# Kernel optimization log

Hardware: AMD Instinct MI355X
Metric: run time of the kernel (lower is better)

## Reference

```python
import jax, jax.numpy as jnp
import numpy as np

N, E, D, H, G, L, EF = 50000, 800000, 128, 256, 512, 3, 8
BN_EPS = 1e-5


def _bn(h, g, b):
    # torch BatchNorm1d in training mode: biased batch stats over the node axis
    m = h.mean(0)
    v = h.var(0)
    return g * (h - m) * jax.lax.rsqrt(v + BN_EPS) + b


def setup_inputs() -> dict:
    ks = jax.random.split(jax.random.key(0), 12)
    sc = 0.05
    return {
        "x": jax.random.normal(ks[0], (N, D), jnp.float32),
        "edge_attr": jax.random.normal(ks[1], (E, EF), jnp.float32),
        "vn_emb": jnp.zeros((1, D), jnp.float32),  # init.constant_(0)
        "We": jax.random.normal(ks[2], (L, EF, D)) * sc,
        "be": jnp.zeros((L, D)),
        "W1": jax.random.normal(ks[3], (L, D, H)) * sc,
        "b1": jnp.zeros((L, H)),
        "g1": jnp.ones((L, H)),
        "bt1": jnp.zeros((L, H)),
        "W2": jax.random.normal(ks[4], (L, H, D)) * sc,
        "b2": jnp.zeros((L, D)),
        "gb": jnp.ones((L, D)),
        "bb": jnp.zeros((L, D)),
        "Wv1": jax.random.normal(ks[5], (L - 1, D, H)) * sc,
        "bv1": jnp.zeros((L - 1, H)),
        "gv1": jnp.ones((L - 1, H)),
        "btv1": jnp.zeros((L - 1, H)),
        "Wv2": jax.random.normal(ks[6], (L - 1, H, D)) * sc,
        "bv2": jnp.zeros((L - 1, D)),
        "gv2": jnp.ones((L - 1, D)),
        "btv2": jnp.zeros((L - 1, D)),
        "edge_index": jax.random.randint(ks[7], (2, E), 0, N),
        "batch": jnp.sort(jax.random.randint(ks[8], (N,), 0, G)),
    }


def reference(x, edge_attr, vn_emb, We, be, W1, b1, g1, bt1, W2, b2, gb, bb,
              Wv1, bv1, gv1, btv1, Wv2, bv2, gv2, btv2, edge_index, batch):
    src, dst = edge_index[0], edge_index[1]
    vn = jnp.broadcast_to(vn_emb, (G, D))  # Embedding(1, D) looked up for every graph
    h = x  # node_encoder is None -> encoded_node = x
    for l in range(L):
        h_in = h + vn[batch]                              # virtual-node broadcast (gather)
        e = edge_attr @ We[l] + be[l]                     # per-layer edge encoder
        msg = jax.nn.relu(h_in[src] + e)                  # GIN message, [E, D]
        aggr = jax.ops.segment_sum(msg, dst, num_segments=N)
        z = h_in + aggr                                   # (1+eps)*h + aggr, eps=0
        z = jax.nn.relu(_bn(z @ W1[l] + b1[l], g1[l], bt1[l]))
        h = _bn(z @ W2[l] + b2[l], gb[l], bb[l])          # conv MLP out + outer BatchNorm
        if l < L - 1:
            h = jax.nn.relu(h)                            # dropout ratio 0 -> identity
            pooled = jax.ops.segment_sum(h_in, batch, num_segments=G) + vn
            t = jax.nn.relu(_bn(pooled @ Wv1[l] + bv1[l], gv1[l], btv1[l]))
            vn = jax.nn.relu(_bn(t @ Wv2[l] + bv2[l], gv2[l], btv2[l]))
    return h  # JK == 'last'
```

## Files before the change

### kernel.cpp

```cpp
#include <hip/hip_runtime.h>
#include <hip/hip_bf16.h>

#define N_NODES 50000
#define N_EDGES 800000
#define DIM 128
#define HID 256
#define N_GRAPH 512
#define N_LAYER 3
#define EFEAT 8
#define BN_EPS 1e-5f
#define MAX_GROUPS 240000
#define AGGR_WAVES 8192
#define SCAN_BLOCKS ((N_NODES + 1023) / 1024)

typedef unsigned short u16;
typedef unsigned int u32;

using bf16x8_t = short __attribute__((ext_vector_type(8)));
using f32x4_t  = float __attribute__((ext_vector_type(4)));
using f32x2    = float __attribute__((ext_vector_type(2)));
using f32x4v   = float __attribute__((ext_vector_type(4)));


__device__ __forceinline__ void atomic_add_f(float* p, float v) {
    unsafeAtomicAdd(p, v);
}
__device__ __forceinline__ u16 f2bf(float x) {
    union { float f; u32 u; } v; v.f = x;
    u32 r = v.u + 0x7FFF + ((v.u >> 16) & 1);
    return (u16)(r >> 16);
}
__device__ __forceinline__ float bf2f(u16 u) {
    union { u32 i; float f; } v; v.i = (u32)u << 16; return v.f;
}
__device__ __forceinline__ float2 up2(u32 p) {
    return make_float2(bf2f((u16)(p & 0xFFFF)), bf2f((u16)(p >> 16)));
}
__device__ __forceinline__ u32 pk2(float a, float b) {
    return (u32)f2bf(a) | ((u32)f2bf(b) << 16);
}
__device__ __forceinline__ f32x2 up2p(u32 p) {
    union { u32 u[2]; f32x2 f; } v;
    v.u[0] = p << 16;
    v.u[1] = p & 0xFFFF0000u;
    return v.f;
}
__device__ __forceinline__ f32x2 splat2(float x) {
    f32x2 r; r.x = x; r.y = x; return r;
}

__global__ __launch_bounds__(256) void wconv_kernel(
    const float* __restrict__ W1, const float* __restrict__ W2,
    u16* __restrict__ W1t, u16* __restrict__ W2t)
{
    int idx = blockIdx.x * 256 + threadIdx.x;
    if (idx >= 6 * 32768) return;
    int m = idx >> 15;
    int off = idx & 32767;
    int l = m >> 1;
    if ((m & 1) == 0) {
        int r = off >> 8, c = off & 255;
        W1t[(size_t)l * 32768 + c * 128 + r] = f2bf(W1[(size_t)l * 32768 + r * 256 + c]);
    } else {
        int r = off >> 7, c = off & 127;
        W2t[(size_t)l * 32768 + c * 256 + r] = f2bf(W2[(size_t)l * 32768 + r * 128 + c]);
    }
}

__global__ __launch_bounds__(256) void hist_rank_kernel(
    const int* __restrict__ ei, int* __restrict__ deg, int* __restrict__ rank)
{
    int e = blockIdx.x * 256 + threadIdx.x;
    if (e >= N_EDGES) return;
    int dst = ei[N_EDGES + e];
    rank[e] = atomicAdd(&deg[dst], 1);
}

__global__ __launch_bounds__(1024) void scan1_kernel(
    const int* __restrict__ deg, int* __restrict__ grpptr, int* __restrict__ bsum)
{
    __shared__ int wsum[16];
    int blk = blockIdx.x, tid = threadIdx.x;
    int i = blk * 1024 + tid;
    int v = (i < N_NODES) ? ((deg[i] + 3) >> 2) : 0;
    int lane = tid & 63, w = tid >> 6;
    int s = v;
    #pragma unroll
    for (int d = 1; d < 64; d <<= 1) { int t = __shfl_up(s, d); if (lane >= d) s += t; }
    if (lane == 63) wsum[w] = s;
    __syncthreads();
    if (tid < 64) {
        int t = (tid < 16) ? wsum[tid] : 0;
        #pragma unroll
        for (int d = 1; d < 16; d <<= 1) { int u = __shfl_up(t, d); if (tid >= d) t += u; }
        if (tid < 16) wsum[tid] = t;
    }
    __syncthreads();
    int excl = (w > 0) ? wsum[w - 1] : 0;
    int incl = s + excl;
    if (i < N_NODES) grpptr[i + 1] = incl;
    if (tid == 1023) bsum[blk] = incl;
}

__global__ __launch_bounds__(64) void scan2_kernel(int* __restrict__ bsum) {
    int tid = threadIdx.x;
    int v = (tid < SCAN_BLOCKS) ? bsum[tid] : 0;
    int s = v;
    #pragma unroll
    for (int d = 1; d < 64; d <<= 1) { int t = __shfl_up(s, d); if (tid >= d) s += t; }
    if (tid < SCAN_BLOCKS) bsum[tid] = s - v;
}

__global__ __launch_bounds__(1024) void scan3_kernel(
    int* __restrict__ grpptr, const int* __restrict__ bsum)
{
    int blk = blockIdx.x;
    int i = blk * 1024 + threadIdx.x;
    if (i < N_NODES) grpptr[i + 1] += bsum[blk];
    if (blk == 0 && threadIdx.x == 0) grpptr[0] = 0;
}

__global__ __launch_bounds__(256) void padinit_kernel(
    uint4* __restrict__ rec4, int nq, u16* __restrict__ hin)
{
    int i = blockIdx.x * 256 + threadIdx.x;
    if (blockIdx.x == 0 && threadIdx.x < 64)
        *(u32*)(hin + (size_t)N_NODES * DIM + threadIdx.x * 2) = 0xFF7FFF7Fu;
    if (i >= nq) return;
    u32 s = (u32)N_NODES << 8;
    rec4[i] = make_uint4(s, 0u, s, 0u);
}

__global__ __launch_bounds__(256) void scatter_kernel(
    const int* __restrict__ ei,
    const int* __restrict__ rank, const int* __restrict__ grpptr,
    uint2* __restrict__ srec)
{
    int e = blockIdx.x * 256 + threadIdx.x;
    if (e >= N_EDGES) return;
    int src = __builtin_nontemporal_load(ei + e);
    int dst = __builtin_nontemporal_load(ei + N_EDGES + e);
    int rk  = __builtin_nontemporal_load(rank + e);
    int slot = (grpptr[dst] + (rk >> 2)) * 4 + (rk & 3);
    uint2 v;
    v.x = (u32)src << 8;
    v.y = (u32)e << 5;
    srec[slot] = v;
}

__global__ __launch_bounds__(256) void expand_kernel(
    const uint2* __restrict__ srec, const float* __restrict__ ea,
    char* __restrict__ brec, int nslots)
{
    int i = blockIdx.x * 256 + threadIdx.x;
    if (i >= nslots) return;
    int g = i >> 2;
    int j = i & 3;
    uint2 v = srec[i];
    const char* eaB = (const char*)ea;
    f32x4v lo = *(const f32x4v*)(eaB + v.y);
    f32x4v hi = *(const f32x4v*)(eaB + v.y + 16);
    char* rb = brec + (size_t)g * 144;
    *(u32*)(rb + j * 4) = v.x;
    *(f32x4v*)(rb + 16 + j * 32) = lo;
    *(f32x4v*)(rb + 32 + j * 32) = hi;
}

__global__ __launch_bounds__(256) void wstart_kernel(
    const int* __restrict__ grpptr, int* __restrict__ wstart)
{
    int w = blockIdx.x * 256 + threadIdx.x;
    if (w > AGGR_WAVES) return;
    if (w == AGGR_WAVES) { wstart[w] = N_NODES; return; }
    int Gt = grpptr[N_NODES];
    int q = (int)(((long long)w * Gt) / AGGR_WAVES);
    int lo = 0, hi = N_NODES;
    while (lo < hi) { int mid = (lo + hi) >> 1; if (grpptr[mid] < q) lo = mid + 1; else hi = mid; }
    wstart[w] = lo;
}

template <bool USEBN, int VNM>
__global__ __launch_bounds__(256) void hin_kernel(
    const float* __restrict__ src,
    const float* __restrict__ sum2, const float* __restrict__ ss2,
    const float* __restrict__ g, const float* __restrict__ b, float invN,
    const int* __restrict__ batch,
    const float* __restrict__ vn_emb,
    const float* __restrict__ vnpre, const float* __restrict__ vsum, const float* __restrict__ vss,
    const float* __restrict__ gv, const float* __restrict__ btv, float invG,
    u16* __restrict__ hin, int total4)
{
    int idx = blockIdx.x * 256 + threadIdx.x;
    if (idx >= total4) return;
    int base = idx * 4;
    int n = base >> 7;
    int c = base & (DIM - 1);
    float4 v = *(const float4*)(src + base);
    float o[4] = {v.x, v.y, v.z, v.w};
    if (USEBN) {
        #pragma unroll
        for (int j = 0; j < 4; ++j) {
            int cj = c + j;
            float m = sum2[cj] * invN;
            float var = ss2[cj] * invN - m * m;
            float r = rsqrtf(var + BN_EPS);
            float a = g[cj] * r;
            o[j] = fmaxf(fmaf(a, o[j], b[cj] - m * a), 0.f);
        }
    }
    int grp = batch[n];
    if (VNM == 0) {
        const float4 w = *(const float4*)(vn_emb + c);
        o[0] += w.x; o[1] += w.y; o[2] += w.z; o[3] += w.w;
    } else {
        const float4 vp = *(const float4*)(vnpre + (size_t)grp * DIM + c);
        float vv[4] = {vp.x, vp.y, vp.z, vp.w};
        #pragma unroll
        for (int j = 0; j < 4; ++j) {
            int cj = c + j;
            float m = vsum[cj] * invG;
            float var = vss[cj] * invG - m * m;
            float r = rsqrtf(var + BN_EPS);
            float a = gv[cj] * r;
            o[j] += fmaxf(fmaf(a, vv[j], btv[cj] - m * a), 0.f);
        }
    }
    uint2 pk;
    pk.x = pk2(o[0], o[1]);
    pk.y = pk2(o[2], o[3]);
    *(uint2*)(hin + base) = pk;
}

__device__ __forceinline__ void edge_term_f(
    u32 h, f32x4v ea, f32x4v eb, const f32x2* rW, f32x2 rB, f32x2& acc)
{
    f32x2 ex = rB;
    ex = __builtin_elementwise_fma(splat2(ea.x), rW[0], ex);
    ex = __builtin_elementwise_fma(splat2(ea.y), rW[1], ex);
    ex = __builtin_elementwise_fma(splat2(ea.z), rW[2], ex);
    ex = __builtin_elementwise_fma(splat2(ea.w), rW[3], ex);
    ex = __builtin_elementwise_fma(splat2(eb.x), rW[4], ex);
    ex = __builtin_elementwise_fma(splat2(eb.y), rW[5], ex);
    ex = __builtin_elementwise_fma(splat2(eb.z), rW[6], ex);
    ex = __builtin_elementwise_fma(splat2(eb.w), rW[7], ex);
    f32x2 s = up2p(h) + ex;
    s = __builtin_elementwise_max(s, splat2(0.f));
    acc += s;
}

__global__ __launch_bounds__(256) void aggr_kernel(
    const int* __restrict__ grpptr, const char* __restrict__ rec,
    const float* __restrict__ Wel, const float* __restrict__ bel,
    const u16* __restrict__ hin, u16* __restrict__ z,
    const int* __restrict__ wstart, float* __restrict__ stats)
{
    const int lane = threadIdx.x & 63;
    const int cb = lane * 4;
    const int wid = __builtin_amdgcn_readfirstlane((blockIdx.x << 2) + (threadIdx.x >> 6));

    if (blockIdx.x == 0) {
        #pragma unroll
        for (int i = 0; i < 8; ++i) stats[i * 256 + threadIdx.x] = 0.f;
    }

    f32x2 rW[EFEAT];
    #pragma unroll
    for (int k = 0; k < EFEAT; ++k) {
        float2 t = *(const float2*)(Wel + k * DIM + lane * 2);
        rW[k].x = t.x; rW[k].y = t.y;
    }
    float2 tb = *(const float2*)(bel + lane * 2);
    f32x2 rB; rB.x = tb.x; rB.y = tb.y;

    const char* hinB = (const char*)hin;
    int n = wstart[wid];
    const int n1 = wstart[wid + 1];

    while (n < n1 && grpptr[n + 1] == grpptr[n]) {
        f32x2 a0 = up2p(*(const u32*)(hinB + ((u32)n << 8) + cb));
        *(u32*)(z + ((size_t)n << 7) + lane * 2) = pk2(a0.x, a0.y);
        ++n;
    }
    if (n < n1) {
        int g = grpptr[n];
        const int gTot = grpptr[n1];
        int gEnd = grpptr[n + 1];
        f32x2 acc = up2p(*(const u32*)(hinB + ((u32)n << 8) + cb));
        const char* rb = rec + (size_t)g * 144;

        uint4 so = *(const uint4*)rb;
        u32 h0 = *(const u32*)(hinB + so.x + cb);
        u32 h1 = *(const u32*)(hinB + so.y + cb);
        u32 h2 = *(const u32*)(hinB + so.z + cb);
        u32 h3 = *(const u32*)(hinB + so.w + cb);
        f32x4v e0a = *(const f32x4v*)(rb + 16);
        f32x4v e0b = *(const f32x4v*)(rb + 32);
        f32x4v e1a = *(const f32x4v*)(rb + 48);
        f32x4v e1b = *(const f32x4v*)(rb + 64);
        f32x4v e2a = *(const f32x4v*)(rb + 80);
        f32x4v e2b = *(const f32x4v*)(rb + 96);
        f32x4v e3a = *(const f32x4v*)(rb + 112);
        f32x4v e3b = *(const f32x4v*)(rb + 128);
        uint4 soN = *(const uint4*)(rb + 144);

        #pragma unroll 2
        for (; g < gTot; ++g, rb += 144) {
            u32 i0 = *(const u32*)(hinB + soN.x + cb);
            u32 i1 = *(const u32*)(hinB + soN.y + cb);
            u32 i2 = *(const u32*)(hinB + soN.z + cb);
            u32 i3 = *(const u32*)(hinB + soN.w + cb);
            f32x4v f0a = *(const f32x4v*)(rb + 160);
            f32x4v f0b = *(const f32x4v*)(rb + 176);
            f32x4v f1a = *(const f32x4v*)(rb + 192);
            f32x4v f1b = *(const f32x4v*)(rb + 208);
            f32x4v f2a = *(const f32x4v*)(rb + 224);
            f32x4v f2b = *(const f32x4v*)(rb + 240);
            f32x4v f3a = *(const f32x4v*)(rb + 256);
            f32x4v f3b = *(const f32x4v*)(rb + 272);
            uint4 soNN = *(const uint4*)(rb + 288);
            edge_term_f(h0, e0a, e0b, rW, rB, acc);
            edge_term_f(h1, e1a, e1b, rW, rB, acc);
            edge_term_f(h2, e2a, e2b, rW, rB, acc);
            edge_term_f(h3, e3a, e3b, rW, rB, acc);
            h0 = i0; h1 = i1; h2 = i2; h3 = i3;
            e0a = f0a; e0b = f0b; e1a = f1a; e1b = f1b;
            e2a = f2a; e2b = f2b; e3a = f3a; e3b = f3b;
            soN = soNN;
            if (g + 1 == gEnd) {
                *(u32*)(z + ((size_t)n << 7) + lane * 2) = pk2(acc.x, acc.y);
                ++n;
                if (g + 1 < gTot) {
                    while (grpptr[n + 1] == grpptr[n]) {
                        f32x2 a0 = up2p(*(const u32*)(hinB + ((u32)n << 8) + cb));
                        *(u32*)(z + ((size_t)n << 7) + lane * 2) = pk2(a0.x, a0.y);
                        ++n;
                    }
                    acc = up2p(*(const u32*)(hinB + ((u32)n << 8) + cb));
                    gEnd = grpptr[n + 1];
                }
            }
        }
    }
    while (n < n1) {
        f32x2 a0 = up2p(*(const u32*)(hinB + ((u32)n << 8) + cb));
        *(u32*)(z + ((size_t)n << 7) + lane * 2) = pk2(a0.x, a0.y);
        ++n;
    }
}

template <int MODE, bool CBF16>
__global__ __launch_bounds__(256) void gemm_bf16_kernel(
    const u16* __restrict__ Aa,
    const float* __restrict__ sSum, const float* __restrict__ sSS,
    const float* __restrict__ gA, const float* __restrict__ btA, float invCnt,
    const u16* __restrict__ Bt,
    const float* __restrict__ bias,
    void* __restrict__ CoutV,
    float* __restrict__ outSum, float* __restrict__ outSS,
    int M, int K, int Nc)
{
    constexpr int BM = 128, BN = 128, BK = 128;
    constexpr int LDA = BK + 8;
    __shared__ u16 As[BM * LDA];
    __shared__ u16 Bs[64 * LDA];
    __shared__ float csum[BN], css[BN];

    const int tid = threadIdx.x;
    const int wave = tid >> 6, lane = tid & 63;
    const int row0 = blockIdx.x * BM, col0 = blockIdx.y * BN;
    const int w_m = (wave & 1) * 64, w_n = (wave >> 1) * 32;
    const int quad = lane >> 4, l16 = lane & 15;

    if (tid < BN) { csum[tid] = 0.f; css[tid] = 0.f; }

    f32x4_t acc[4][4];
    #pragma unroll
    for (int mi = 0; mi < 4; ++mi)
        #pragma unroll
        for (int ni = 0; ni < 4; ++ni)
            acc[mi][ni] = (f32x4_t){0.f, 0.f, 0.f, 0.f};

    const int kc = (tid & 15) * 8;
    const int nkt = K / BK;

    for (int kt = 0; kt < nkt; ++kt) {
        float af[8], bf_[8];
        if (MODE == 1) {
            #pragma unroll
            for (int j = 0; j < 8; ++j) {
                int kg = kt * BK + kc + j;
                float m = sSum[kg] * invCnt;
                float var = sSS[kg] * invCnt - m * m;
                float r = rsqrtf(var + BN_EPS);
                float a = gA[kg] * r;
                af[j] = a;
                bf_[j] = btA[kg] - m * a;
            }
        }
        #pragma unroll
        for (int it = 0; it < 8; ++it) {
            int chunk = it * 256 + tid;
            int row = chunk >> 4;
            int gr = row0 + row; if (gr >= M) gr = M - 1;
            uint4 q = *(const uint4*)(Aa + (size_t)gr * K + kt * BK + kc);
            if (MODE == 1) {
                float2 p0 = up2(q.x), p1 = up2(q.y), p2 = up2(q.z), p3 = up2(q.w);
                p0.x = fmaxf(fmaf(af[0], p0.x, bf_[0]), 0.f);
                p0.y = fmaxf(fmaf(af[1], p0.y, bf_[1]), 0.f);
                p1.x = fmaxf(fmaf(af[2], p1.x, bf_[2]), 0.f);
                p1.y = fmaxf(fmaf(af[3], p1.y, bf_[3]), 0.f);
                p2.x = fmaxf(fmaf(af[4], p2.x, bf_[4]), 0.f);
                p2.y = fmaxf(fmaf(af[5], p2.y, bf_[5]), 0.f);
                p3.x = fmaxf(fmaf(af[6], p3.x, bf_[6]), 0.f);
                p3.y = fmaxf(fmaf(af[7], p3.y, bf_[7]), 0.f);
                q.x = pk2(p0.x, p0.y); q.y = pk2(p1.x, p1.y);
                q.z = pk2(p2.x, p2.y); q.w = pk2(p3.x, p3.y);
            }
            *(uint4*)(As + row * LDA + kc) = q;
        }
        #pragma unroll
        for (int half = 0; half < 2; ++half) {
            #pragma unroll
            for (int it = 0; it < 4; ++it) {
                int chunk = it * 256 + tid;
                int n = chunk >> 4;
                uint4 q = *(const uint4*)(Bt + (size_t)(col0 + half * 64 + n) * K + kt * BK + kc);
                *(uint4*)(Bs + n * LDA + kc) = q;
            }
            __syncthreads();
            #pragma unroll
            for (int ks = 0; ks < 4; ++ks) {
                bf16x8_t a_frag[4], b_frag[2];
                #pragma unroll
                for (int mi = 0; mi < 4; ++mi)
                    a_frag[mi] = *(const bf16x8_t*)(As + (w_m + mi * 16 + l16) * LDA + ks * 32 + quad * 8);
                #pragma unroll
                for (int ni = 0; ni < 2; ++ni)
                    b_frag[ni] = *(const bf16x8_t*)(Bs + (w_n + ni * 16 + l16) * LDA + ks * 32 + quad * 8);
                #pragma unroll
                for (int mi = 0; mi < 4; ++mi)
                    #pragma unroll
                    for (int ni = 0; ni < 2; ++ni)
                        acc[mi][half * 2 + ni] = __builtin_amdgcn_mfma_f32_16x16x32_bf16(
                            a_frag[mi], b_frag[ni], acc[mi][half * 2 + ni], 0, 0, 0);
            }
            __syncthreads();
        }
    }

    u16* Cb = (u16*)CoutV;
    float* Cf = (float*)CoutV;
    #pragma unroll
    for (int half = 0; half < 2; ++half)
    #pragma unroll
    for (int ni = 0; ni < 2; ++ni) {
        int ccol = half * 64 + w_n + ni * 16 + l16;
        int col = col0 + ccol;
        float bv = bias[col];
        float s = 0.f, qs = 0.f;
        #pragma unroll
        for (int mi = 0; mi < 4; ++mi) {
            int rbase = row0 + w_m + mi * 16 + quad * 4;
            #pragma unroll
            for (int reg = 0; reg < 4; ++reg) {
                int gr = rbase + reg;
                if (gr < M) {
                    float o = acc[mi][half * 2 + ni][reg] + bv;
                    s += o;
                    qs += o * o;
                    if (CBF16) Cb[(size_t)gr * Nc + col] = f2bf(o);
                    else       Cf[(size_t)gr * Nc + col] = o;
                }
            }
        }
        s += __shfl_xor(s, 16);  s += __shfl_xor(s, 32);
        qs += __shfl_xor(qs, 16);  qs += __shfl_xor(qs, 32);
        if (quad == 0) {
            atomicAdd(&csum[ccol], s);
            atomicAdd(&css[ccol], qs);
        }
    }
    __syncthreads();
    if (tid < BN) {
        atomic_add_f(outSum + col0 + tid, csum[tid]);
        atomic_add_f(outSS + col0 + tid, css[tid]);
    }
}

template <int MODE>
__global__ __launch_bounds__(256) void gemm_kernel(
    const float* __restrict__ Aa,
    const float* __restrict__ sSum, const float* __restrict__ sSS,
    const float* __restrict__ gA, const float* __restrict__ btA, float invCnt,
    const float* __restrict__ B, const float* __restrict__ bias,
    float* __restrict__ Cout, float* __restrict__ outSum, float* __restrict__ outSS,
    int M, int K, int Nc)
{
    __shared__ float As[16][68];
    __shared__ float Bs[16][64];
    __shared__ float alphaS[256], betaS[256];
    __shared__ float csum[64], css[64];

    const int tid = threadIdx.x;
    const int tx = tid & 15, ty = tid >> 4;
    const int row0 = blockIdx.x * 64, col0 = blockIdx.y * 64;

    if (tid < 64) { csum[tid] = 0.f; css[tid] = 0.f; }
    if (MODE == 1) {
        for (int k = tid; k < K; k += 256) {
            float m = sSum[k] * invCnt;
            float var = sSS[k] * invCnt - m * m;
            float r = rsqrtf(var + BN_EPS);
            float a = gA[k] * r;
            alphaS[k] = a;
            betaS[k] = btA[k] - m * a;
        }
    }
    __syncthreads();

    float acc[4][4];
    #pragma unroll
    for (int i = 0; i < 4; ++i)
        #pragma unroll
        for (int j = 0; j < 4; ++j) acc[i][j] = 0.f;

    const int lr = tid >> 2;
    const int lk = (tid & 3) * 4;
    const int bk = tid >> 4;
    const int bc = tx * 4;

    for (int kt = 0; kt < K; kt += 16) {
        int gr = row0 + lr;
        float4 va = make_float4(0.f, 0.f, 0.f, 0.f);
        if (gr < M) {
            va = *(const float4*)(Aa + (size_t)gr * K + kt + lk);
            if (MODE == 1) {
                int k0 = kt + lk;
                va.x = fmaxf(fmaf(alphaS[k0 + 0], va.x, betaS[k0 + 0]), 0.f);
                va.y = fmaxf(fmaf(alphaS[k0 + 1], va.y, betaS[k0 + 1]), 0.f);
                va.z = fmaxf(fmaf(alphaS[k0 + 2], va.z, betaS[k0 + 2]), 0.f);
                va.w = fmaxf(fmaf(alphaS[k0 + 3], va.w, betaS[k0 + 3]), 0.f);
            }
        }
        As[lk + 0][lr] = va.x;
        As[lk + 1][lr] = va.y;
        As[lk + 2][lr] = va.z;
        As[lk + 3][lr] = va.w;
        const float4 vb4 = *(const float4*)(B + (size_t)(kt + bk) * Nc + col0 + bc);
        *(float4*)&Bs[bk][bc] = vb4;
        __syncthreads();
        #pragma unroll
        for (int kk = 0; kk < 16; ++kk) {
            const float4 a4 = *(const float4*)&As[kk][ty * 4];
            const float4 b4 = *(const float4*)&Bs[kk][tx * 4];
            float av[4] = {a4.x, a4.y, a4.z, a4.w};
            float bv4[4] = {b4.x, b4.y, b4.z, b4.w};
            #pragma unroll
            for (int i = 0; i < 4; ++i)
                #pragma unroll
                for (int j = 0; j < 4; ++j)
                    acc[i][j] = fmaf(av[i], bv4[j], acc[i][j]);
        }
        __syncthreads();
    }

    const float4 bvv = *(const float4*)(bias + col0 + tx * 4);
    float bias4[4] = {bvv.x, bvv.y, bvv.z, bvv.w};
    float ps[4] = {0.f, 0.f, 0.f, 0.f};
    float pq[4] = {0.f, 0.f, 0.f, 0.f};
    #pragma unroll
    for (int i = 0; i < 4; ++i) {
        int gr = row0 + ty * 4 + i;
        if (gr < M) {
            float o[4];
            #pragma unroll
            for (int j = 0; j < 4; ++j) {
                o[j] = acc[i][j] + bias4[j];
                ps[j] += o[j];
                pq[j] += o[j] * o[j];
            }
            *(float4*)(Cout + (size_t)gr * Nc + col0 + tx * 4) = make_float4(o[0], o[1], o[2], o[3]);
        }
    }
    #pragma unroll
    for (int j = 0; j < 4; ++j) {
        atomicAdd(&csum[tx * 4 + j], ps[j]);
        atomicAdd(&css[tx * 4 + j], pq[j]);
    }
    __syncthreads();
    if (tid < 64) {
        atomic_add_f(outSum + col0 + tid, csum[tid]);
        atomic_add_f(outSS + col0 + tid, css[tid]);
    }
}

template <int VNM>
__global__ __launch_bounds__(64) void pooled_seg_kernel(
    const u16* __restrict__ hin, const int* __restrict__ batch,
    const float* __restrict__ vn_emb,
    const float* __restrict__ vnpre, const float* __restrict__ vsum, const float* __restrict__ vss,
    const float* __restrict__ gv, const float* __restrict__ btv, float invG,
    float* __restrict__ pooled)
{
    int g = blockIdx.x;
    int lane = threadIdx.x;
    int c2 = lane * 2;
    int lo = 0, hi = N_NODES;
    while (lo < hi) { int mid = (lo + hi) >> 1; if (batch[mid] < g) lo = mid + 1; else hi = mid; }
    int start = lo;
    hi = N_NODES;
    while (lo < hi) { int mid = (lo + hi) >> 1; if (batch[mid] < g + 1) lo = mid + 1; else hi = mid; }
    int end = lo;

    f32x2 acc;
    if (VNM == 0) {
        float2 w = *(const float2*)(vn_emb + c2);
        acc.x = w.x; acc.y = w.y;
    } else {
        float2 vs = *(const float2*)(vsum + c2);
        float2 vq = *(const float2*)(vss + c2);
        float2 gg = *(const float2*)(gv + c2);
        float2 bt = *(const float2*)(btv + c2);
        float2 vp = *(const float2*)(vnpre + (size_t)g * DIM + c2);
        float m0 = vs.x * invG, m1 = vs.y * invG;
        float va0 = vq.x * invG - m0 * m0, va1 = vq.y * invG - m1 * m1;
        float a0 = gg.x * rsqrtf(va0 + BN_EPS), a1 = gg.y * rsqrtf(va1 + BN_EPS);
        acc.x = fmaxf(fmaf(a0, vp.x, bt.x - m0 * a0), 0.f);
        acc.y = fmaxf(fmaf(a1, vp.y, bt.y - m1 * a1), 0.f);
    }

    const char* hinB = (const char*)hin;
    const int cb = lane * 4;
    f32x2 s0 = splat2(0.f), s1 = splat2(0.f), s2 = splat2(0.f), s3 = splat2(0.f);
    int n = start;
    for (; n + 3 < end; n += 4) {
        s0 += up2p(*(const u32*)(hinB + ((size_t)(n + 0) << 8) + cb));
        s1 += up2p(*(const u32*)(hinB + ((size_t)(n + 1) << 8) + cb));
        s2 += up2p(*(const u32*)(hinB + ((size_t)(n + 2) << 8) + cb));
        s3 += up2p(*(const u32*)(hinB + ((size_t)(n + 3) << 8) + cb));
    }
    for (; n < end; ++n) s0 += up2p(*(const u32*)(hinB + ((size_t)n << 8) + cb));
    acc += (s0 + s1) + (s2 + s3);
    *(float2*)(pooled + (size_t)g * DIM + c2) = make_float2(acc.x, acc.y);
}

__global__ __launch_bounds__(256) void final_bn_kernel(
    float* __restrict__ outp, const float* __restrict__ sum2, const float* __restrict__ ss2,
    const float* __restrict__ g, const float* __restrict__ b, float invN, int total4)
{
    int idx = blockIdx.x * 256 + threadIdx.x;
    if (idx >= total4) return;
    int base = idx * 4;
    int c = base & (DIM - 1);
    float4 v = *(const float4*)(outp + base);
    float o[4] = {v.x, v.y, v.z, v.w};
    #pragma unroll
    for (int j = 0; j < 4; ++j) {
        int cj = c + j;
        float m = sum2[cj] * invN;
        float var = ss2[cj] * invN - m * m;
        float r = rsqrtf(var + BN_EPS);
        float a = g[cj] * r;
        o[j] = fmaf(a, o[j], b[cj] - m * a);
    }
    *(float4*)(outp + base) = make_float4(o[0], o[1], o[2], o[3]);
}

extern "C" void kernel_launch(void* const* d_in, const int* in_sizes, int n_in,
                              void* d_out, int out_size, void* d_ws, size_t ws_size,
                              hipStream_t stream) {
    const float* x         = (const float*)d_in[0];
    const float* edge_attr = (const float*)d_in[1];
    const float* vn_emb    = (const float*)d_in[2];
    const float* We        = (const float*)d_in[3];
    const float* be        = (const float*)d_in[4];
    const float* W1        = (const float*)d_in[5];
    const float* b1        = (const float*)d_in[6];
    const float* g1v       = (const float*)d_in[7];
    const float* bt1       = (const float*)d_in[8];
    const float* W2        = (const float*)d_in[9];
    const float* b2        = (const float*)d_in[10];
    const float* gb        = (const float*)d_in[11];
    const float* bb        = (const float*)d_in[12];
    const float* Wv1       = (const float*)d_in[13];
    const float* bv1       = (const float*)d_in[14];
    const float* gv1       = (const float*)d_in[15];
    const float* btv1      = (const float*)d_in[16];
    const float* Wv2       = (const float*)d_in[17];
    const float* bv2       = (const float*)d_in[18];
    const float* gv2       = (const float*)d_in[19];
    const float* btv2      = (const float*)d_in[20];
    const int* edge_index  = (const int*)d_in[21];
    const int* batch       = (const int*)d_in[22];
    float* outp = (float*)d_out;

    auto au = [](size_t x) { return (x + 255) & ~(size_t)255; };
    char* p = (char*)d_ws;
    u16* h_in   = (u16*)p;  p += au((size_t)(N_NODES + 1) * DIM * 2);
    u16* z_bf   = (u16*)p;  p += au((size_t)N_NODES * DIM * 2);
    u16* c1_bf  = (u16*)p;  p += au((size_t)N_NODES * HID * 2);
    u16* W1t    = (u16*)p;  p += au((size_t)3 * 32768 * 2);
    u16* W2t    = (u16*)p;  p += au((size_t)3 * 32768 * 2);
    float* pooled = (float*)p;  p += au((size_t)N_GRAPH * DIM * 4);
    float* tpre   = (float*)p;  p += au((size_t)N_GRAPH * HID * 4);
    float* vnpre  = (float*)p;  p += au((size_t)N_GRAPH * DIM * 4);
    float* stats  = (float*)p;  p += au(2048 * 4);
    float* sum1 = stats,        *ss1 = stats + 256;
    float* sum2 = stats + 512,  *ss2 = stats + 640;
    float* vsum1 = stats + 768, *vss1 = stats + 1024;
    float* vsum2 = stats + 1280, *vss2 = stats + 1408;
    int* grpptr = (int*)p;  p += au((size_t)(N_NODES + 1) * 4);
    int* wstart = (int*)p;  p += au((size_t)(AGGR_WAVES + 1) * 4);
    int* bsum   = (int*)p;  p += au((size_t)SCAN_BLOCKS * 4);
    char* brec  = p;        p += au((size_t)(MAX_GROUPS + 4) * 144 + 512);
    int* deg   = (int*)z_bf;
    int* rank  = (int*)c1_bf;
    uint2* srec = (uint2*)(c1_bf + au((size_t)N_EDGES * 4) / 2);

    const float invN = 1.0f / (float)N_NODES;
    const float invG = 1.0f / (float)N_GRAPH;
    const int total4 = N_NODES * DIM / 4;
    const int nslots = (MAX_GROUPS + 4) * 4;

    hipMemsetAsync(deg, 0, N_NODES * sizeof(int), stream);
    hist_rank_kernel<<<(N_EDGES + 255) / 256, 256, 0, stream>>>(edge_index, deg, rank);
    scan1_kernel<<<SCAN_BLOCKS, 1024, 0, stream>>>(deg, grpptr, bsum);
    scan2_kernel<<<1, 64, 0, stream>>>(bsum);
    scan3_kernel<<<SCAN_BLOCKS, 1024, 0, stream>>>(grpptr, bsum);
    padinit_kernel<<<(nslots / 2 + 255) / 256, 256, 0, stream>>>((uint4*)srec, nslots / 2, h_in);
    scatter_kernel<<<(N_EDGES + 255) / 256, 256, 0, stream>>>(
        edge_index, rank, grpptr, srec);
    expand_kernel<<<(nslots + 255) / 256, 256, 0, stream>>>(
        srec, edge_attr, brec, nslots);
    wstart_kernel<<<(AGGR_WAVES + 256) / 256, 256, 0, stream>>>(grpptr, wstart);
    wconv_kernel<<<768, 256, 0, stream>>>(W1, W2, W1t, W2t);

    const int AGGR_BLOCKS = AGGR_WAVES / 4;

    for (int l = 0; l < N_LAYER; ++l) {
        if (l == 0)
            hin_kernel<false, 0><<<(total4 + 255) / 256, 256, 0, stream>>>(
                x, nullptr, nullptr, nullptr, nullptr, 0.f, batch,
                vn_emb, nullptr, nullptr, nullptr, nullptr, nullptr, 0.f,
                h_in, total4);
        else
            hin_kernel<true, 1><<<(total4 + 255) / 256, 256, 0, stream>>>(
                outp, sum2, ss2, gb + (size_t)(l - 1) * DIM, bb + (size_t)(l - 1) * DIM, invN, batch,
                nullptr, vnpre, vsum2, vss2,
                gv2 + (size_t)(l - 1) * DIM, btv2 + (size_t)(l - 1) * DIM, invG,
                h_in, total4);

        if (l == 0)
            pooled_seg_kernel<0><<<N_GRAPH, 64, 0, stream>>>(
                h_in, batch, vn_emb, nullptr, nullptr, nullptr, nullptr, nullptr, 0.f, pooled);
        else if (l < N_LAYER - 1)
            pooled_seg_kernel<1><<<N_GRAPH, 64, 0, stream>>>(
                h_in, batch, nullptr, vnpre, vsum2, vss2,
                gv2 + (size_t)(l - 1) * DIM, btv2 + (size_t)(l - 1) * DIM, invG, pooled);

        aggr_kernel<<<AGGR_BLOCKS, 256, 0, stream>>>(
            grpptr, brec, We + (size_t)l * EFEAT * DIM, be + (size_t)l * DIM,
            h_in, z_bf, wstart, stats);

        dim3 g1d((N_NODES + 127) / 128, HID / 128);
        gemm_bf16_kernel<0, true><<<g1d, 256, 0, stream>>>(
            z_bf, nullptr, nullptr, nullptr, nullptr, 0.f,
            W1t + (size_t)l * 32768, b1 + (size_t)l * HID,
            (void*)c1_bf, sum1, ss1, N_NODES, DIM, HID);

        dim3 g2d((N_NODES + 127) / 128, DIM / 128);
        gemm_bf16_kernel<1, false><<<g2d, 256, 0, stream>>>(
            c1_bf, sum1, ss1, g1v + (size_t)l * HID, bt1 + (size_t)l * HID, invN,
            W2t + (size_t)l * 32768, b2 + (size_t)l * DIM,
            (void*)outp, sum2, ss2, N_NODES, HID, DIM);

        if (l < N_LAYER - 1) {
            dim3 g3d(N_GRAPH / 64, HID / 64);
            gemm_kernel<0><<<g3d, 256, 0, stream>>>(
                pooled, nullptr, nullptr, nullptr, nullptr, 0.f,
                Wv1 + (size_t)l * DIM * HID, bv1 + (size_t)l * HID,
                tpre, vsum1, vss1, N_GRAPH, DIM, HID);

            dim3 g4d(N_GRAPH / 64, DIM / 64);
            gemm_kernel<1><<<g4d, 256, 0, stream>>>(
                tpre, vsum1, vss1, gv1 + (size_t)l * HID, btv1 + (size_t)l * HID, invG,
                Wv2 + (size_t)l * HID * DIM, bv2 + (size_t)l * DIM,
                vnpre, vsum2, vss2, N_GRAPH, HID, DIM);
        }
    }

    final_bn_kernel<<<(total4 + 255) / 256, 256, 0, stream>>>(
        outp, sum2, ss2, gb + (size_t)2 * DIM, bb + (size_t)2 * DIM, invN, total4);
}
```

Measured before the change: 732.2 us.

## Replace tiled bf16 GEMMs with weight-resident streaming GEMM reading A directly

Swaps the LDS-tiled 128x128 bf16 GEMM for a kernel that keeps the whole weight slice in LDS and lets each wave stream a 32-row A tile straight from global memory into MFMA fragments. The BatchNorm scale and shift for the second GEMM are computed once per block into LDS rather than per k-tile per thread. The aim is to drop the A staging through LDS and the per-tile barriers. In exchange A is loaded without LDS reuse, and the second GEMM now splits its columns into two 64-wide blocks, so each A row is read twice.

```diff
diff --git a/kernel.cpp b/kernel.cpp
--- a/kernel.cpp
+++ b/kernel.cpp
@@ -348,8 +348,27 @@
     }
 }
 
-template <int MODE, bool CBF16>
-__global__ __launch_bounds__(256) void gemm_bf16_kernel(
+__device__ __forceinline__ bf16x8_t bn_relu8(
+    bf16x8_t a, int k0, const float* __restrict__ alphaS, const float* __restrict__ betaS)
+{
+    union { bf16x8_t v; u32 u[4]; } in, out;
+    in.v = a;
+    #pragma unroll
+    for (int j = 0; j < 4; ++j) {
+        f32x2 x = up2p(in.u[j]);
+        float2 al = *(const float2*)(alphaS + k0 + j * 2);
+        float2 be = *(const float2*)(betaS + k0 + j * 2);
+        f32x2 av; av.x = al.x; av.y = al.y;
+        f32x2 bv; bv.x = be.x; bv.y = be.y;
+        f32x2 r = __builtin_elementwise_fma(x, av, bv);
+        r = __builtin_elementwise_max(r, splat2(0.f));
+        out.u[j] = pk2(r.x, r.y);
+    }
+    return out.v;
+}
+
+template <int MODE, bool CBF16, int K, int NCB>
+__global__ __launch_bounds__(256) void gemm_stream_kernel(
     const u16* __restrict__ Aa,
     const float* __restrict__ sSum, const float* __restrict__ sSS,
     const float* __restrict__ gA, const float* __restrict__ btA, float invCnt,
@@ -357,133 +376,113 @@
     const float* __restrict__ bias,
     void* __restrict__ CoutV,
     float* __restrict__ outSum, float* __restrict__ outSS,
-    int M, int K, int Nc)
-{
-    constexpr int BM = 128, BN = 128, BK = 128;
-    constexpr int LDA = BK + 8;
-    __shared__ u16 As[BM * LDA];
-    __shared__ u16 Bs[64 * LDA];
-    __shared__ float csum[BN], css[BN];
+    int M, int Nc)
+{
+    constexpr int LDK = K + 8;
+    constexpr int NT = NCB / 16;
+    constexpr int KS = K / 32;
+    constexpr int TPR = K / 8;
+    constexpr int NLOAD = NCB * TPR / 256;
+    __shared__ u16 Bs[NCB * LDK];
+    __shared__ float alphaS[K], betaS[K];
+    __shared__ float csum[NCB], css[NCB];
 
     const int tid = threadIdx.x;
     const int wave = tid >> 6, lane = tid & 63;
-    const int row0 = blockIdx.x * BM, col0 = blockIdx.y * BN;
-    const int w_m = (wave & 1) * 64, w_n = (wave >> 1) * 32;
     const int quad = lane >> 4, l16 = lane & 15;
-
-    if (tid < BN) { csum[tid] = 0.f; css[tid] = 0.f; }
-
-    f32x4_t acc[4][4];
-    #pragma unroll
-    for (int mi = 0; mi < 4; ++mi)
-        #pragma unroll
-        for (int ni = 0; ni < 4; ++ni)
-            acc[mi][ni] = (f32x4_t){0.f, 0.f, 0.f, 0.f};
-
-    const int kc = (tid & 15) * 8;
-    const int nkt = K / BK;
-
-    for (int kt = 0; kt < nkt; ++kt) {
-        float af[8], bf_[8];
-        if (MODE == 1) {
+    const int col0 = blockIdx.y * NCB;
+
+    #pragma unroll
+    for (int i = tid; i < NCB; i += 256) { csum[i] = 0.f; css[i] = 0.f; }
+    if (MODE == 1) {
+        for (int k = tid; k < K; k += 256) {
+            float m = sSum[k] * invCnt;
+            float var = sSS[k] * invCnt - m * m;
+            float r = rsqrtf(var + BN_EPS);
+            float a = gA[k] * r;
+            alphaS[k] = a;
+            betaS[k] = btA[k] - m * a;
+        }
+    }
+    #pragma unroll
+    for (int it = 0; it < NLOAD; ++it) {
+        int chunk = it * 256 + tid;
+        int nrow = chunk / TPR;
+        int k0 = (chunk % TPR) * 8;
+        uint4 q = *(const uint4*)(Bt + (size_t)(col0 + nrow) * K + k0);
+        *(uint4*)(Bs + nrow * LDK + k0) = q;
+    }
+    __syncthreads();
+
+    const int ntile = (M + 31) >> 5;
+    const int wtile = blockIdx.x * 4 + wave;
+    if (wtile < ntile) {
+        const int m0 = wtile * 32;
+        int ra = m0 + l16;       if (ra >= M) ra = M - 1;
+        int rb = m0 + 16 + l16;  if (rb >= M) rb = M - 1;
+        const u16* A0 = Aa + (size_t)ra * K;
+        const u16* A1 = Aa + (size_t)rb * K;
+
+        f32x4_t acc[2][NT];
+        #pragma unroll
+        for (int s = 0; s < 2; ++s)
             #pragma unroll
-            for (int j = 0; j < 8; ++j) {
-                int kg = kt * BK + kc + j;
-                float m = sSum[kg] * invCnt;
-                float var = sSS[kg] * invCnt - m * m;
-                float r = rsqrtf(var + BN_EPS);
-                float a = gA[kg] * r;
-                af[j] = a;
-                bf_[j] = btA[kg] - m * a;
+            for (int ni = 0; ni < NT; ++ni)
+                acc[s][ni] = (f32x4_t){0.f, 0.f, 0.f, 0.f};
+
+        #pragma unroll
+        for (int ks = 0; ks < KS; ++ks) {
+            const int k0 = ks * 32 + quad * 8;
+            bf16x8_t a0 = *(const bf16x8_t*)(A0 + k0);
+            bf16x8_t a1 = *(const bf16x8_t*)(A1 + k0);
+            if (MODE == 1) {
+                a0 = bn_relu8(a0, k0, alphaS, betaS);
+                a1 = bn_relu8(a1, k0, alphaS, betaS);
             }
-        }
-        #pragma unroll
-        for (int it = 0; it < 8; ++it) {
-            int chunk = it * 256 + tid;
-            int row = chunk >> 4;
-            int gr = row0 + row; if (gr >= M) gr = M - 1;
-            uint4 q = *(const uint4*)(Aa + (size_t)gr * K + kt * BK + kc);
-            if (MODE == 1) {
-                float2 p0 = up2(q.x), p1 = up2(q.y), p2 = up2(q.z), p3 = up2(q.w);
-                p0.x = fmaxf(fmaf(af[0], p0.x, bf_[0]), 0.f);
-                p0.y = fmaxf(fmaf(af[1], p0.y, bf_[1]), 0.f);
-                p1.x = fmaxf(fmaf(af[2], p1.x, bf_[2]), 0.f);
-                p1.y = fmaxf(fmaf(af[3], p1.y, bf_[3]), 0.f);
-                p2.x = fmaxf(fmaf(af[4], p2.x, bf_[4]), 0.f);
-                p2.y = fmaxf(fmaf(af[5], p2.y, bf_[5]), 0.f);
-                p3.x = fmaxf(fmaf(af[6], p3.x, bf_[6]), 0.f);
-                p3.y = fmaxf(fmaf(af[7], p3.y, bf_[7]), 0.f);
-                q.x = pk2(p0.x, p0.y); q.y = pk2(p1.x, p1.y);
-                q.z = pk2(p2.x, p2.y); q.w = pk2(p3.x, p3.y);
+            #pragma unroll
+            for (int ni = 0; ni < NT; ++ni) {
+                bf16x8_t b = *(const bf16x8_t*)(Bs + (ni * 16 + l16) * LDK + k0);
+                acc[0][ni] = __builtin_amdgcn_mfma_f32_16x16x32_bf16(a0, b, acc[0][ni], 0, 0, 0);
+                acc[1][ni] = __builtin_amdgcn_mfma_f32_16x16x32_bf16(a1, b, acc[1][ni], 0, 0, 0);
             }
-            *(uint4*)(As + row * LDA + kc) = q;
-        }
-        #pragma unroll
-        for (int half = 0; half < 2; ++half) {
+        }
+
+        u16* Cb = (u16*)CoutV;
+        float* Cf = (float*)CoutV;
+        #pragma unroll
+        for (int ni = 0; ni < NT; ++ni) {
+            int lc = ni * 16 + l16;
+            int col = col0 + lc;
+            float bv = bias[col];
+            float s = 0.f, qs = 0.f;
             #pragma unroll
-            for (int it = 0; it < 4; ++it) {
-                int chunk = it * 256 + tid;
-                int n = chunk >> 4;
-                uint4 q = *(const uint4*)(Bt + (size_t)(col0 + half * 64 + n) * K + kt * BK + kc);
-                *(uint4*)(Bs + n * LDA + kc) = q;
-            }
-            __syncthreads();
-            #pragma unroll
-            for (int ks = 0; ks < 4; ++ks) {
-                bf16x8_t a_frag[4], b_frag[2];
+            for (int sub = 0; sub < 2; ++sub) {
+                int rbase = m0 + sub * 16 + quad * 4;
                 #pragma unroll
-                for (int mi = 0; mi < 4; ++mi)
-                    a_frag[mi] = *(const bf16x8_t*)(As + (w_m + mi * 16 + l16) * LDA + ks * 32 + quad * 8);
-                #pragma unroll
-                for (int ni = 0; ni < 2; ++ni)
-                    b_frag[ni] = *(const bf16x8_t*)(Bs + (w_n + ni * 16 + l16) * LDA + ks * 32 + quad * 8);
-                #pragma unroll
-                for (int mi = 0; mi < 4; ++mi)
-                    #pragma unroll
-                    for (int ni = 0; ni < 2; ++ni)
-                        acc[mi][half * 2 + ni] = __builtin_amdgcn_mfma_f32_16x16x32_bf16(
-                            a_frag[mi], b_frag[ni], acc[mi][half * 2 + ni], 0, 0, 0);
-            }
-            __syncthreads();
-        }
-    }
-
-    u16* Cb = (u16*)CoutV;
-    float* Cf = (float*)CoutV;
-    #pragma unroll
-    for (int half = 0; half < 2; ++half)
-    #pragma unroll
-    for (int ni = 0; ni < 2; ++ni) {
-        int ccol = half * 64 + w_n + ni * 16 + l16;
-        int col = col0 + ccol;
-        float bv = bias[col];
-        float s = 0.f, qs = 0.f;
-        #pragma unroll
-        for (int mi = 0; mi < 4; ++mi) {
-            int rbase = row0 + w_m + mi * 16 + quad * 4;
-            #pragma unroll
-            for (int reg = 0; reg < 4; ++reg) {
-                int gr = rbase + reg;
-                if (gr < M) {
-                    float o = acc[mi][half * 2 + ni][reg] + bv;
-                    s += o;
-                    qs += o * o;
-                    if (CBF16) Cb[(size_t)gr * Nc + col] = f2bf(o);
-                    else       Cf[(size_t)gr * Nc + col] = o;
+                for (int reg = 0; reg < 4; ++reg) {
+                    int gr = rbase + reg;
+                    if (gr < M) {
+                        float o = acc[sub][ni][reg] + bv;
+                        s += o;
+                        qs += o * o;
+                        if (CBF16) Cb[(size_t)gr * Nc + col] = f2bf(o);
+                        else       Cf[(size_t)gr * Nc + col] = o;
+                    }
                 }
             }
-        }
-        s += __shfl_xor(s, 16);  s += __shfl_xor(s, 32);
-        qs += __shfl_xor(qs, 16);  qs += __shfl_xor(qs, 32);
-        if (quad == 0) {
-            atomicAdd(&csum[ccol], s);
-            atomicAdd(&css[ccol], qs);
+            s += __shfl_xor(s, 16);  s += __shfl_xor(s, 32);
+            qs += __shfl_xor(qs, 16);  qs += __shfl_xor(qs, 32);
+            if (quad == 0) {
+                atomicAdd(&csum[lc], s);
+                atomicAdd(&css[lc], qs);
+            }
         }
     }
     __syncthreads();
-    if (tid < BN) {
-        atomic_add_f(outSum + col0 + tid, csum[tid]);
-        atomic_add_f(outSS + col0 + tid, css[tid]);
+    #pragma unroll
+    for (int i = tid; i < NCB; i += 256) {
+        atomic_add_f(outSum + col0 + i, csum[i]);
+        atomic_add_f(outSS + col0 + i, css[i]);
     }
 }
 
@@ -736,6 +735,8 @@
     wconv_kernel<<<768, 256, 0, stream>>>(W1, W2, W1t, W2t);
 
     const int AGGR_BLOCKS = AGGR_WAVES / 4;
+    const int ntile32 = (N_NODES + 31) / 32;
+    const int gsx = (ntile32 + 3) / 4;
 
     for (int l = 0; l < N_LAYER; ++l) {
         if (l == 0)
@@ -762,17 +763,17 @@
             grpptr, brec, We + (size_t)l * EFEAT * DIM, be + (size_t)l * DIM,
             h_in, z_bf, wstart, stats);
 
-        dim3 g1d((N_NODES + 127) / 128, HID / 128);
-        gemm_bf16_kernel<0, true><<<g1d, 256, 0, stream>>>(
+        dim3 g1d(gsx, HID / 128);
+        gemm_stream_kernel<0, true, DIM, 128><<<g1d, 256, 0, stream>>>(
             z_bf, nullptr, nullptr, nullptr, nullptr, 0.f,
             W1t + (size_t)l * 32768, b1 + (size_t)l * HID,
-            (void*)c1_bf, sum1, ss1, N_NODES, DIM, HID);
-
-        dim3 g2d((N_NODES + 127) / 128, DIM / 128);
-        gemm_bf16_kernel<1, false><<<g2d, 256, 0, stream>>>(
+            (void*)c1_bf, sum1, ss1, N_NODES, HID);
+
+        dim3 g2d(gsx, DIM / 64);
+        gemm_stream_kernel<1, false, HID, 64><<<g2d, 256, 0, stream>>>(
             c1_bf, sum1, ss1, g1v + (size_t)l * HID, bt1 + (size_t)l * HID, invN,
             W2t + (size_t)l * 32768, b2 + (size_t)l * DIM,
-            (void*)outp, sum2, ss2, N_NODES, HID, DIM);
+            (void*)outp, sum2, ss2, N_NODES, DIM);
 
         if (l < N_LAYER - 1) {
             dim3 g3d(N_GRAPH / 64, HID / 64);
```

Result: faster. 707.1 us (-3.4%).
